# Kernel optimization log

Measured on AMD Instinct MI355X. Metric: run time of the kernel, lower is better.

The kernel has to match this reference:

```python
import jax, jax.numpy as jnp
import numpy as np

L = 28; D = 1024; HQ = 16; HKV = 8; HD = 128; G = HQ // HKV
FF = 3072; VOCAB = 151936; THETA = 1000000.0; EPS = 1e-6
B = 2; PAST = 1024
SCALE = HD ** -0.5


def _rmsnorm(x, w):
    v = jnp.mean(jnp.square(x), axis=-1, keepdims=True)
    return x * jax.lax.rsqrt(v + EPS) * w


def _rotate_half(x):
    x1, x2 = jnp.split(x, 2, axis=-1)
    return jnp.concatenate([-x2, x1], axis=-1)


def setup_inputs() -> dict:
    key = jax.random.key(0)
    ks = jax.random.split(key, 12)
    s = 0.02
    return {
        "input_embeds": jax.random.normal(ks[0], (B, 1, D), jnp.float32),
        "position_ids": jax.random.randint(ks[1], (B, 1), 0, PAST).astype(jnp.int32),
        "past_keys": jax.random.normal(ks[2], (L, B, HKV, PAST, HD), jnp.float32),
        "past_values": jax.random.normal(ks[3], (L, B, HKV, PAST, HD), jnp.float32),
        "Wq": s * jax.random.normal(ks[4], (L, D, HQ * HD), jnp.float32),
        "Wk": s * jax.random.normal(ks[5], (L, D, HKV * HD), jnp.float32),
        "Wv": s * jax.random.normal(ks[6], (L, D, HKV * HD), jnp.float32),
        "Wo": s * jax.random.normal(ks[7], (L, HQ * HD, D), jnp.float32),
        "Wg": s * jax.random.normal(ks[8], (L, D, FF), jnp.float32),
        "Wu": s * jax.random.normal(ks[9], (L, D, FF), jnp.float32),
        "Wd": s * jax.random.normal(ks[10], (L, FF, D), jnp.float32),
        "ln1_w": jnp.ones((L, D), jnp.float32),
        "ln2_w": jnp.ones((L, D), jnp.float32),
        "qn_w": jnp.ones((L, HD), jnp.float32),
        "kn_w": jnp.ones((L, HD), jnp.float32),
        "final_norm_w": jnp.ones((D,), jnp.float32),
        "lm_head_w": s * jax.random.normal(ks[11], (D, VOCAB), jnp.float32),
    }


def reference(input_embeds, position_ids, past_keys, past_values,
              Wq, Wk, Wv, Wo, Wg, Wu, Wd,
              ln1_w, ln2_w, qn_w, kn_w, final_norm_w, lm_head_w):
    # Rotary embeddings for the single new position.
    pos = position_ids.astype(jnp.float32)                      # [B,1]
    inv_freq = 1.0 / (THETA ** (jnp.arange(0, HD, 2, dtype=jnp.float32) / HD))
    freqs = pos[..., None] * inv_freq                           # [B,1,HD/2]
    emb = jnp.concatenate([freqs, freqs], axis=-1)              # [B,1,HD]
    cos = jnp.cos(emb)[:, None, :, :]                           # [B,1,1,HD] (head bcast)
    sin = jnp.sin(emb)[:, None, :, :]

    def layer(h, xs):
        wq, wk, wv, wo, wg, wu, wd, l1, l2, qw, kw, pk, pv = xs
        n = _rmsnorm(h, l1)                                     # [B,1,D]
        q = _rmsnorm((n @ wq).reshape(B, 1, HQ, HD), qw).transpose(0, 2, 1, 3)   # [B,HQ,1,HD]
        k = _rmsnorm((n @ wk).reshape(B, 1, HKV, HD), kw).transpose(0, 2, 1, 3)  # [B,HKV,1,HD]
        v = (n @ wv).reshape(B, 1, HKV, HD).transpose(0, 2, 1, 3)
        q = q * cos + _rotate_half(q) * sin
        k = k * cos + _rotate_half(k) * sin
        K = jnp.concatenate([pk, k], axis=2)                    # [B,HKV,PAST+1,HD]
        V = jnp.concatenate([pv, v], axis=2)
        # GQA without materializing repeated KV: q heads grouped kv-major,
        # matching torch _repeat_kv head ordering (head = kv*G + g).
        qg = q[:, :, 0, :].reshape(B, HKV, G, HD)
        scores = jnp.einsum('bkgd,bksd->bkgs', qg, K) * SCALE
        w = jax.nn.softmax(scores.astype(jnp.float32), axis=-1).astype(q.dtype)
        o = jnp.einsum('bkgs,bksd->bkgd', w, V).reshape(B, 1, HQ * HD)
        h = h + o @ wo
        m = _rmsnorm(h, l2)
        h = h + (jax.nn.silu(m @ wg) * (m @ wu)) @ wd           # SwiGLU MLP
        return h, (K, V)

    xs = (Wq, Wk, Wv, Wo, Wg, Wu, Wd, ln1_w, ln2_w, qn_w, kn_w, past_keys, past_values)
    h, (present_keys, present_values) = jax.lax.scan(layer, input_embeds, xs)
    logits = _rmsnorm(h, final_norm_w) @ lm_head_w              # [B,1,VOCAB]
    return logits, present_keys, present_values
```

## Files before the change

### kernel.cpp

```cpp
#include <hip/hip_runtime.h>
#include <math.h>

#define NL 28
#define DIM 1024
#define NHQ 16
#define NHKV 8
#define HDIM 128
#define NG 2
#define NFF 3072
#define NVOCAB 151936
#define NB 2
#define NPAST 1024
#define NPTOT 1025
#define EPSF 1e-6f
#define QKSCALE 0.08838834764831845f
#define LOGTHETA 13.815510557964274f

#define SQKV 8
#define SCH 32

#define OFF_N1   0
#define OFF_H    2048
#define OFF_H1   4096
#define OFF_QKV  8192
#define OFF_AM   73728
#define OFF_AL   74752
#define OFF_AO   75776
#define OFF_WO   206848
#define OFF_G    223232
#define OFF_U    272384
#define OFF_WD   321536

#define PK_OFF ((size_t)NB*NVOCAB)
#define PV_OFF (PK_OFF + (size_t)NL*NB*NHKV*NPTOT*HDIM)

__global__ __launch_bounds__(256) void k0_init(const float* __restrict__ embeds,
    const float* __restrict__ ln1, float* __restrict__ ws)
{
  int tid = threadIdx.x;
  __shared__ float red[512];
  int d = tid*4;
  float4 v0 = *(const float4*)(embeds + d);
  float4 v1 = *(const float4*)(embeds + DIM + d);
  *(float4*)(ws + OFF_H + d) = v0;
  *(float4*)(ws + OFF_H + DIM + d) = v1;
  red[tid]     = v0.x*v0.x + v0.y*v0.y + v0.z*v0.z + v0.w*v0.w;
  red[256+tid] = v1.x*v1.x + v1.y*v1.y + v1.z*v1.z + v1.w*v1.w;
  __syncthreads();
  for (int off = 128; off > 0; off >>= 1) {
    if (tid < off) { red[tid] += red[tid+off]; red[256+tid] += red[256+tid+off]; }
    __syncthreads();
  }
  float r0 = rsqrtf(red[0]/DIM + EPSF);
  float r1 = rsqrtf(red[256]/DIM + EPSF);
  float4 w = *(const float4*)(ln1 + d);
  float4 n0 = make_float4(v0.x*r0*w.x, v0.y*r0*w.y, v0.z*r0*w.z, v0.w*r0*w.w);
  float4 n1 = make_float4(v1.x*r1*w.x, v1.y*r1*w.y, v1.z*r1*w.z, v1.w*r1*w.w);
  *(float4*)(ws + OFF_N1 + d) = n0;
  *(float4*)(ws + OFF_N1 + DIM + d) = n1;
}

__global__ __launch_bounds__(256) void k1_qkv(
    const float* __restrict__ Wq_, const float* __restrict__ Wk_,
    const float* __restrict__ Wv_, const float* __restrict__ ln1,
    float* __restrict__ ws, int l)
{
  int bx = blockIdx.x, by = blockIdx.y;
  int tid = threadIdx.x;
  __shared__ __align__(16) float sh[NB][128];
  __shared__ __align__(16) float red[256*9];

  int ct = tid & 15, rs = tid >> 4;
  int colg = bx*64 + ct*4;
  const float* W; int O; int wcol;
  if (bx < 32)      { W = Wq_; O = 2048; wcol = colg; }
  else if (bx < 48) { W = Wk_; O = 1024; wcol = colg - 2048; }
  else              { W = Wv_; O = 1024; wcol = colg - 3072; }
  int r0 = rs*8;
  const float* Wp = W + (size_t)l*DIM*O + (size_t)(by*128 + r0)*O + wcol;
  float4 wb[8];
  #pragma unroll
  for (int i = 0; i < 8; i++) wb[i] = *(const float4*)(Wp + (size_t)i*O);

  if (l == 0) {
    int b = tid >> 7, r = tid & 127;
    sh[b][r] = ws[OFF_N1 + b*DIM + by*128 + r];
    __syncthreads();
  } else {
    int d = tid*4;
    float4 a0 = *(const float4*)(ws + OFF_H1 + d);
    float4 a1 = *(const float4*)(ws + OFF_H1 + DIM + d);
    #pragma unroll
    for (int s = 0; s < 8; s++) {
      float4 p0 = *(const float4*)(ws + OFF_WD + (s*NB + 0)*DIM + d);
      float4 p1 = *(const float4*)(ws + OFF_WD + (s*NB + 1)*DIM + d);
      a0.x += p0.x; a0.y += p0.y; a0.z += p0.z; a0.w += p0.w;
      a1.x += p1.x; a1.y += p1.y; a1.z += p1.z; a1.w += p1.w;
    }
    if (bx == 0 && by == 0) {
      *(float4*)(ws + OFF_H + d) = a0;
      *(float4*)(ws + OFF_H + DIM + d) = a1;
    }
    red[tid]     = a0.x*a0.x + a0.y*a0.y + a0.z*a0.z + a0.w*a0.w;
    red[256+tid] = a1.x*a1.x + a1.y*a1.y + a1.z*a1.z + a1.w*a1.w;
    __syncthreads();
    for (int off = 128; off > 0; off >>= 1) {
      if (tid < off) { red[tid] += red[tid+off]; red[256+tid] += red[256+tid+off]; }
      __syncthreads();
    }
    float rq0 = rsqrtf(red[0]/DIM + EPSF);
    float rq1 = rsqrtf(red[256]/DIM + EPSF);
    float4 lw = *(const float4*)(ln1 + (size_t)l*DIM + d);
    int r = d - by*128;
    if (r >= 0 && r < 128) {
      sh[0][r] = a0.x*rq0*lw.x; sh[0][r+1] = a0.y*rq0*lw.y;
      sh[0][r+2] = a0.z*rq0*lw.z; sh[0][r+3] = a0.w*rq0*lw.w;
      sh[1][r] = a1.x*rq1*lw.x; sh[1][r+1] = a1.y*rq1*lw.y;
      sh[1][r+2] = a1.z*rq1*lw.z; sh[1][r+3] = a1.w*rq1*lw.w;
    }
    __syncthreads();
  }

  float a[2][4] = {};
  #pragma unroll
  for (int i = 0; i < 8; i++) {
    float x0 = sh[0][r0+i], x1 = sh[1][r0+i];
    a[0][0] += x0*wb[i].x; a[0][1] += x0*wb[i].y; a[0][2] += x0*wb[i].z; a[0][3] += x0*wb[i].w;
    a[1][0] += x1*wb[i].x; a[1][1] += x1*wb[i].y; a[1][2] += x1*wb[i].z; a[1][3] += x1*wb[i].w;
  }
  float* rp = red + tid*9;
  #pragma unroll
  for (int e = 0; e < 4; e++) { rp[e] = a[0][e]; rp[4+e] = a[1][e]; }
  __syncthreads();
  if (tid < 16) {
    float o[8] = {};
    #pragma unroll
    for (int j = 0; j < 16; j++) {
      const float* q = red + (size_t)(j*16 + tid)*9;
      #pragma unroll
      for (int e = 0; e < 8; e++) o[e] += q[e];
    }
    int cg = bx*64 + tid*4;
    #pragma unroll
    for (int e = 0; e < 4; e++) {
      ws[OFF_QKV + (by*NB + 0)*4096 + cg + e] = o[e];
      ws[OFF_QKV + (by*NB + 1)*4096 + cg + e] = o[4+e];
    }
  }
}

__global__ __launch_bounds__(256) void k2_attn(
    const float* __restrict__ pastK, const float* __restrict__ pastV,
    const int* __restrict__ posids, const float* __restrict__ qnw,
    const float* __restrict__ knw, float* __restrict__ out,
    float* __restrict__ ws, int l)
{
  int c = blockIdx.x, kv = blockIdx.y, b = blockIdx.z;
  int tid = threadIdx.x;
  __shared__ __align__(16) float qf[NG][HDIM];
  __shared__ __align__(16) float kf[HDIM];
  __shared__ __align__(16) float vf[HDIM];
  __shared__ __align__(16) float pre[3*HDIM];
  __shared__ __align__(16) float po[8][NG][HDIM];
  __shared__ float red[256];
  __shared__ float pm[8][NG], pl[8][NG];

  int g = tid >> 7, o = tid & 127;
  int hq = kv*NG + g;
  float qraw = 0.f, kvraw = 0.f;
  #pragma unroll
  for (int s = 0; s < SQKV; s++) qraw += ws[OFF_QKV + (s*NB + b)*4096 + hq*HDIM + o];
  if (g == 0) {
    #pragma unroll
    for (int s = 0; s < SQKV; s++) kvraw += ws[OFF_QKV + (s*NB + b)*4096 + 2048 + kv*HDIM + o];
  } else {
    #pragma unroll
    for (int s = 0; s < SQKV; s++) kvraw += ws[OFF_QKV + (s*NB + b)*4096 + 3072 + kv*HDIM + o];
  }
  red[tid] = qraw*qraw;
  __syncthreads();
  for (int off = 64; off > 0; off >>= 1) {
    if (o < off) red[tid] += red[tid+off];
    __syncthreads();
  }
  float qr = rsqrtf(red[g*128]/HDIM + EPSF);
  __syncthreads();
  red[tid] = (g == 0) ? kvraw*kvraw : 0.f;
  __syncthreads();
  for (int off = 128; off > 0; off >>= 1) {
    if (tid < off) red[tid] += red[tid+off];
    __syncthreads();
  }
  float kr = rsqrtf(red[0]/HDIM + EPSF);
  pre[g*HDIM + o] = qraw*qr*qnw[l*HDIM + o];
  if (g == 0) pre[2*HDIM + o] = kvraw*kr*knw[l*HDIM + o];
  else vf[o] = kvraw;
  __syncthreads();
  float pos = (float)posids[b];
  int j = o & 63;
  float ang = pos * expf(-(2.0f*(float)j/(float)HDIM)*LOGTHETA);
  float sn, cs;
  sincosf(ang, &sn, &cs);
  {
    float qv = pre[g*HDIM + o];
    float qo = (o < 64) ? -pre[g*HDIM + o + 64] : pre[g*HDIM + o - 64];
    qf[g][o] = qv*cs + qo*sn;
    if (g == 0) {
      float kx = pre[2*HDIM + o];
      float ko = (o < 64) ? -pre[2*HDIM + o + 64] : pre[2*HDIM + o - 64];
      kf[o] = kx*cs + ko*sn;
    }
  }
  __syncthreads();

  int lane = tid & 63, w = tid >> 6;
  int h = (lane >> 5) & 1, q = lane & 31;
  int grp = w*2 + h;
  int p0 = c*32;
  int p1 = (c == SCH-1) ? NPTOT : p0 + 32;
  size_t pastbase = ((((size_t)l*NB + b)*NHKV + kv)*NPAST)*HDIM;
  size_t presbase = ((((size_t)l*NB + b)*NHKV + kv)*NPTOT)*HDIM;
  float4 q0 = *(const float4*)&qf[0][q*4];
  float4 q1 = *(const float4*)&qf[1][q*4];
  float sc0[5], sc1[5];
  float4 vv[5];
  int ns = 0;
  for (int p = p0 + grp; p < p1; p += 8) {
    float4 k4, v4;
    if (p < NPAST) {
      k4 = *(const float4*)(pastK + pastbase + (size_t)p*HDIM + q*4);
      v4 = *(const float4*)(pastV + pastbase + (size_t)p*HDIM + q*4);
    } else {
      k4 = *(const float4*)&kf[q*4];
      v4 = *(const float4*)&vf[q*4];
    }
    *(float4*)(out + PK_OFF + presbase + (size_t)p*HDIM + q*4) = k4;
    *(float4*)(out + PV_OFF + presbase + (size_t)p*HDIM + q*4) = v4;
    float d0 = q0.x*k4.x + q0.y*k4.y + q0.z*k4.z + q0.w*k4.w;
    float d1 = q1.x*k4.x + q1.y*k4.y + q1.z*k4.z + q1.w*k4.w;
    #pragma unroll
    for (int off = 16; off > 0; off >>= 1) {
      d0 += __shfl_xor(d0, off);
      d1 += __shfl_xor(d1, off);
    }
    sc0[ns] = d0*QKSCALE; sc1[ns] = d1*QKSCALE; vv[ns] = v4; ns++;
  }
  float m0 = -1e30f, m1 = -1e30f;
  for (int i = 0; i < ns; i++) { m0 = fmaxf(m0, sc0[i]); m1 = fmaxf(m1, sc1[i]); }
  if (q == 0) { pm[grp][0] = m0; pm[grp][1] = m1; }
  __syncthreads();
  float M0 = -1e30f, M1 = -1e30f;
  #pragma unroll
  for (int i = 0; i < 8; i++) { M0 = fmaxf(M0, pm[i][0]); M1 = fmaxf(M1, pm[i][1]); }
  float l0 = 0.f, l1 = 0.f;
  float4 o0 = {0,0,0,0}, o1 = {0,0,0,0};
  for (int i = 0; i < ns; i++) {
    float w0 = __expf(sc0[i] - M0), w1 = __expf(sc1[i] - M1);
    l0 += w0; l1 += w1;
    o0.x += w0*vv[i].x; o0.y += w0*vv[i].y; o0.z += w0*vv[i].z; o0.w += w0*vv[i].w;
    o1.x += w1*vv[i].x; o1.y += w1*vv[i].y; o1.z += w1*vv[i].z; o1.w += w1*vv[i].w;
  }
  if (q == 0) { pl[grp][0] = l0; pl[grp][1] = l1; }
  *(float4*)&po[grp][0][q*4] = o0;
  *(float4*)&po[grp][1][q*4] = o1;
  __syncthreads();
  {
    int head = tid >> 7, dd = tid & 127;
    float acc = 0.f;
    #pragma unroll
    for (int i = 0; i < 8; i++) acc += po[i][head][dd];
    int base = ((b*NHKV + kv)*NG + head)*SCH + c;
    ws[OFF_AO + (size_t)base*HDIM + dd] = acc;
    if (dd == 0) {
      float ll = 0.f;
      #pragma unroll
      for (int i = 0; i < 8; i++) ll += pl[i][head];
      ws[OFF_AM + base] = (head ? M1 : M0);
      ws[OFF_AL + base] = ll;
    }
  }
}

__global__ __launch_bounds__(256) void k3_wo(const float* __restrict__ Wo_,
    float* __restrict__ ws, int l)
{
  int bx = blockIdx.x, by = blockIdx.y;
  int tid = threadIdx.x;
  __shared__ __align__(16) float x[NB][256];
  __shared__ float wf[NB][2][SCH];
  __shared__ float invL[NB][2];
  __shared__ __align__(16) float red[256*9];

  int ct = tid & 7, rs = tid >> 3;
  int col = bx*32 + ct*4;
  int r0 = rs*8;
  const float* Wp = Wo_ + (size_t)l*(NHQ*HDIM)*DIM + (size_t)(by*256 + r0)*DIM + col;
  float4 wb[8];
  #pragma unroll
  for (int i = 0; i < 8; i++) wb[i] = *(const float4*)(Wp + (size_t)i*DIM);

  if (tid < 4) {
    int b = tid >> 1, hh = tid & 1;
    int hb = b*16 + by*2 + hh;
    const float* mp = ws + OFF_AM + hb*SCH;
    const float* lp = ws + OFF_AL + hb*SCH;
    float M = -1e30f;
    for (int cc = 0; cc < SCH; cc++) M = fmaxf(M, mp[cc]);
    float L = 0.f;
    for (int cc = 0; cc < SCH; cc++) { float f = __expf(mp[cc]-M); wf[b][hh][cc] = f; L += lp[cc]*f; }
    invL[b][hh] = 1.0f/L;
  }
  __syncthreads();
  for (int e = tid; e < 512; e += 256) {
    int b = e >> 8, rr = e & 255, hh = rr >> 7, dd = rr & 127;
    int hb = b*16 + by*2 + hh;
    const float* op = ws + OFF_AO + (size_t)(hb*SCH)*HDIM + dd;
    float acc = 0.f;
    for (int cc = 0; cc < SCH; cc++) acc += op[(size_t)cc*HDIM]*wf[b][hh][cc];
    x[b][rr] = acc*invL[b][hh];
  }
  __syncthreads();
  float a[2][4] = {};
  #pragma unroll
  for (int i = 0; i < 8; i++) {
    float x0 = x[0][r0+i], x1 = x[1][r0+i];
    a[0][0] += x0*wb[i].x; a[0][1] += x0*wb[i].y; a[0][2] += x0*wb[i].z; a[0][3] += x0*wb[i].w;
    a[1][0] += x1*wb[i].x; a[1][1] += x1*wb[i].y; a[1][2] += x1*wb[i].z; a[1][3] += x1*wb[i].w;
  }
  float* rp = red + tid*9;
  #pragma unroll
  for (int e = 0; e < 4; e++) { rp[e] = a[0][e]; rp[4+e] = a[1][e]; }
  __syncthreads();
  if (tid < 8) {
    float o[8] = {};
    #pragma unroll
    for (int j = 0; j < 32; j++) {
      const float* qq = red + (size_t)(j*8 + tid)*9;
      #pragma unroll
      for (int e = 0; e < 8; e++) o[e] += qq[e];
    }
    int cg = bx*32 + tid*4;
    #pragma unroll
    for (int e = 0; e < 4; e++) {
      ws[OFF_WO + (by*NB + 0)*DIM + cg + e] = o[e];
      ws[OFF_WO + (by*NB + 1)*DIM + cg + e] = o[4+e];
    }
  }
}

__global__ __launch_bounds__(256) void k4_mlp1(const float* __restrict__ Wg_,
    const float* __restrict__ Wu_, const float* __restrict__ ln2,
    float* __restrict__ ws, int l)
{
  int bx = blockIdx.x, by = blockIdx.y;
  int tid = threadIdx.x;
  __shared__ __align__(16) float sh[NB][128];
  __shared__ __align__(16) float red[256*9];

  int ct = tid & 15, rs = tid >> 4;
  int col = bx*64 + ct*4;
  int r0 = rs*8;
  const float* Wgp = Wg_ + (size_t)l*DIM*NFF + (size_t)(by*128 + r0)*NFF + col;
  const float* Wup = Wu_ + (size_t)l*DIM*NFF + (size_t)(by*128 + r0)*NFF + col;
  float4 wg[8], wu[8];
  #pragma unroll
  for (int i = 0; i < 8; i++) {
    wg[i] = *(const float4*)(Wgp + (size_t)i*NFF);
    wu[i] = *(const float4*)(Wup + (size_t)i*NFF);
  }

  int d = tid*4;
  float4 a0 = *(const float4*)(ws + OFF_H + d);
  float4 a1 = *(const float4*)(ws + OFF_H + DIM + d);
  #pragma unroll
  for (int s = 0; s < 8; s++) {
    float4 p0 = *(const float4*)(ws + OFF_WO + (s*NB + 0)*DIM + d);
    float4 p1 = *(const float4*)(ws + OFF_WO + (s*NB + 1)*DIM + d);
    a0.x += p0.x; a0.y += p0.y; a0.z += p0.z; a0.w += p0.w;
    a1.x += p1.x; a1.y += p1.y; a1.z += p1.z; a1.w += p1.w;
  }
  if (bx == 0 && by == 0) {
    *(float4*)(ws + OFF_H1 + d) = a0;
    *(float4*)(ws + OFF_H1 + DIM + d) = a1;
  }
  red[tid]     = a0.x*a0.x + a0.y*a0.y + a0.z*a0.z + a0.w*a0.w;
  red[256+tid] = a1.x*a1.x + a1.y*a1.y + a1.z*a1.z + a1.w*a1.w;
  __syncthreads();
  for (int off = 128; off > 0; off >>= 1) {
    if (tid < off) { red[tid] += red[tid+off]; red[256+tid] += red[256+tid+off]; }
    __syncthreads();
  }
  float rq0 = rsqrtf(red[0]/DIM + EPSF);
  float rq1 = rsqrtf(red[256]/DIM + EPSF);
  float4 lw = *(const float4*)(ln2 + (size_t)l*DIM + d);
  int r = d - by*128;
  if (r >= 0 && r < 128) {
    sh[0][r] = a0.x*rq0*lw.x; sh[0][r+1] = a0.y*rq0*lw.y;
    sh[0][r+2] = a0.z*rq0*lw.z; sh[0][r+3] = a0.w*rq0*lw.w;
    sh[1][r] = a1.x*rq1*lw.x; sh[1][r+1] = a1.y*rq1*lw.y;
    sh[1][r+2] = a1.z*rq1*lw.z; sh[1][r+3] = a1.w*rq1*lw.w;
  }
  __syncthreads();

  float ag[2][4] = {}, au[2][4] = {};
  #pragma unroll
  for (int i = 0; i < 8; i++) {
    float x0 = sh[0][r0+i], x1 = sh[1][r0+i];
    ag[0][0] += x0*wg[i].x; ag[0][1] += x0*wg[i].y; ag[0][2] += x0*wg[i].z; ag[0][3] += x0*wg[i].w;
    ag[1][0] += x1*wg[i].x; ag[1][1] += x1*wg[i].y; ag[1][2] += x1*wg[i].z; ag[1][3] += x1*wg[i].w;
    au[0][0] += x0*wu[i].x; au[0][1] += x0*wu[i].y; au[0][2] += x0*wu[i].z; au[0][3] += x0*wu[i].w;
    au[1][0] += x1*wu[i].x; au[1][1] += x1*wu[i].y; au[1][2] += x1*wu[i].z; au[1][3] += x1*wu[i].w;
  }
  float* rp = red + tid*9;
  #pragma unroll
  for (int e = 0; e < 4; e++) { rp[e] = ag[0][e]; rp[4+e] = ag[1][e]; }
  __syncthreads();
  if (tid < 16) {
    float o[8] = {};
    #pragma unroll
    for (int j = 0; j < 16; j++) {
      const float* qq = red + (size_t)(j*16 + tid)*9;
      #pragma unroll
      for (int e = 0; e < 8; e++) o[e] += qq[e];
    }
    int cg = bx*64 + tid*4;
    #pragma unroll
    for (int e = 0; e < 4; e++) {
      ws[OFF_G + (by*NB + 0)*NFF + cg + e] = o[e];
      ws[OFF_G + (by*NB + 1)*NFF + cg + e] = o[4+e];
    }
  }
  __syncthreads();
  #pragma unroll
  for (int e = 0; e < 4; e++) { rp[e] = au[0][e]; rp[4+e] = au[1][e]; }
  __syncthreads();
  if (tid < 16) {
    float o[8] = {};
    #pragma unroll
    for (int j = 0; j < 16; j++) {
      const float* qq = red + (size_t)(j*16 + tid)*9;
      #pragma unroll
      for (int e = 0; e < 8; e++) o[e] += qq[e];
    }
    int cg = bx*64 + tid*4;
    #pragma unroll
    for (int e = 0; e < 4; e++) {
      ws[OFF_U + (by*NB + 0)*NFF + cg + e] = o[e];
      ws[OFF_U + (by*NB + 1)*NFF + cg + e] = o[4+e];
    }
  }
}

__global__ __launch_bounds__(256) void k5_mlp2(const float* __restrict__ Wd_,
    float* __restrict__ ws, int l)
{
  int bx = blockIdx.x, by = blockIdx.y;
  int tid = threadIdx.x;
  __shared__ __align__(16) float act[NB][384];
  __shared__ __align__(16) float red[256*9];

  int ct = tid & 7, rs = tid >> 3;
  int col = bx*32 + ct*4;
  int r0 = rs*12;
  const float* Wp = Wd_ + (size_t)l*NFF*DIM + (size_t)(by*384 + r0)*DIM + col;
  float4 wb[12];
  #pragma unroll
  for (int i = 0; i < 12; i++) wb[i] = *(const float4*)(Wp + (size_t)i*DIM);

  for (int e = tid; e < 768; e += 256) {
    int b = (e >= 384);
    int loc = e - b*384;
    int ff = by*384 + loc;
    float g = 0.f, u = 0.f;
    #pragma unroll
    for (int s = 0; s < 8; s++) {
      g += ws[OFF_G + (s*NB + b)*NFF + ff];
      u += ws[OFF_U + (s*NB + b)*NFF + ff];
    }
    act[b][loc] = (g / (1.0f + __expf(-g)))*u;
  }
  __syncthreads();
  float a[2][4] = {};
  #pragma unroll
  for (int i = 0; i < 12; i++) {
    float x0 = act[0][r0+i], x1 = act[1][r0+i];
    a[0][0] += x0*wb[i].x; a[0][1] += x0*wb[i].y; a[0][2] += x0*wb[i].z; a[0][3] += x0*wb[i].w;
    a[1][0] += x1*wb[i].x; a[1][1] += x1*wb[i].y; a[1][2] += x1*wb[i].z; a[1][3] += x1*wb[i].w;
  }
  float* rp = red + tid*9;
  #pragma unroll
  for (int e = 0; e < 4; e++) { rp[e] = a[0][e]; rp[4+e] = a[1][e]; }
  __syncthreads();
  if (tid < 8) {
    float o[8] = {};
    #pragma unroll
    for (int j = 0; j < 32; j++) {
      const float* qq = red + (size_t)(j*8 + tid)*9;
      #pragma unroll
      for (int e = 0; e < 8; e++) o[e] += qq[e];
    }
    int cg = bx*32 + tid*4;
    #pragma unroll
    for (int e = 0; e < 4; e++) {
      ws[OFF_WD + (by*NB + 0)*DIM + cg + e] = o[e];
      ws[OFF_WD + (by*NB + 1)*DIM + cg + e] = o[4+e];
    }
  }
}

__global__ __launch_bounds__(256) void k6_lmhead(const float* __restrict__ lmw,
    const float* __restrict__ fnw, const float* __restrict__ ws,
    float* __restrict__ out)
{
  __shared__ __align__(16) float nf[NB*DIM];
  __shared__ __align__(16) float red[256*9];
  int tid = threadIdx.x;
  int d = tid*4;
  float4 a0 = *(const float4*)(ws + OFF_H1 + d);
  float4 a1 = *(const float4*)(ws + OFF_H1 + DIM + d);
  #pragma unroll
  for (int s = 0; s < 8; s++) {
    float4 p0 = *(const float4*)(ws + OFF_WD + (s*NB + 0)*DIM + d);
    float4 p1 = *(const float4*)(ws + OFF_WD + (s*NB + 1)*DIM + d);
    a0.x += p0.x; a0.y += p0.y; a0.z += p0.z; a0.w += p0.w;
    a1.x += p1.x; a1.y += p1.y; a1.z += p1.z; a1.w += p1.w;
  }
  red[tid]     = a0.x*a0.x + a0.y*a0.y + a0.z*a0.z + a0.w*a0.w;
  red[256+tid] = a1.x*a1.x + a1.y*a1.y + a1.z*a1.z + a1.w*a1.w;
  __syncthreads();
  for (int off = 128; off > 0; off >>= 1) {
    if (tid < off) { red[tid] += red[tid+off]; red[256+tid] += red[256+tid+off]; }
    __syncthreads();
  }
  float rq0 = rsqrtf(red[0]/DIM + EPSF);
  float rq1 = rsqrtf(red[256]/DIM + EPSF);
  float4 fw = *(const float4*)(fnw + d);
  nf[d]   = a0.x*rq0*fw.x; nf[d+1] = a0.y*rq0*fw.y;
  nf[d+2] = a0.z*rq0*fw.z; nf[d+3] = a0.w*rq0*fw.w;
  nf[DIM+d]   = a1.x*rq1*fw.x; nf[DIM+d+1] = a1.y*rq1*fw.y;
  nf[DIM+d+2] = a1.z*rq1*fw.z; nf[DIM+d+3] = a1.w*rq1*fw.w;
  __syncthreads();

  int ct = tid & 15, rs = tid >> 4;
  int col = blockIdx.x*64 + ct*4;
  const float* Wp = lmw + (size_t)(rs*64)*NVOCAB + col;
  float a[2][4] = {};
  for (int t = 0; t < 8; t++) {
    float4 wb[8];
    #pragma unroll
    for (int i = 0; i < 8; i++)
      wb[i] = *(const float4*)(Wp + (size_t)(t*8 + i)*NVOCAB);
    #pragma unroll
    for (int i = 0; i < 8; i++) {
      int rr = rs*64 + t*8 + i;
      float x0 = nf[rr], x1 = nf[DIM+rr];
      a[0][0] += x0*wb[i].x; a[0][1] += x0*wb[i].y; a[0][2] += x0*wb[i].z; a[0][3] += x0*wb[i].w;
      a[1][0] += x1*wb[i].x; a[1][1] += x1*wb[i].y; a[1][2] += x1*wb[i].z; a[1][3] += x1*wb[i].w;
    }
  }
  float* rp = red + tid*9;
  #pragma unroll
  for (int e = 0; e < 4; e++) { rp[e] = a[0][e]; rp[4+e] = a[1][e]; }
  __syncthreads();
  if (tid < 16) {
    float o[8] = {};
    #pragma unroll
    for (int j = 0; j < 16; j++) {
      const float* qq = red + (size_t)(j*16 + tid)*9;
      #pragma unroll
      for (int e = 0; e < 8; e++) o[e] += qq[e];
    }
    int cg = blockIdx.x*64 + tid*4;
    #pragma unroll
    for (int e = 0; e < 4; e++) {
      out[cg + e] = o[e];
      out[NVOCAB + cg + e] = o[4+e];
    }
  }
}

extern "C" void kernel_launch(void* const* d_in, const int* in_sizes, int n_in,
                              void* d_out, int out_size, void* d_ws, size_t ws_size,
                              hipStream_t stream) {
  (void)in_sizes; (void)n_in; (void)out_size; (void)ws_size;
  const float* embeds = (const float*)d_in[0];
  const int*   posids = (const int*)d_in[1];
  const float* pastK  = (const float*)d_in[2];
  const float* pastV  = (const float*)d_in[3];
  const float* Wq     = (const float*)d_in[4];
  const float* Wk     = (const float*)d_in[5];
  const float* Wv     = (const float*)d_in[6];
  const float* Wo     = (const float*)d_in[7];
  const float* Wg     = (const float*)d_in[8];
  const float* Wu     = (const float*)d_in[9];
  const float* Wd     = (const float*)d_in[10];
  const float* ln1    = (const float*)d_in[11];
  const float* ln2    = (const float*)d_in[12];
  const float* qnw    = (const float*)d_in[13];
  const float* knw    = (const float*)d_in[14];
  const float* fnw    = (const float*)d_in[15];
  const float* lmw    = (const float*)d_in[16];
  float* out = (float*)d_out;
  float* ws  = (float*)d_ws;

  k0_init<<<1, 256, 0, stream>>>(embeds, ln1, ws);
  for (int l = 0; l < NL; l++) {
    k1_qkv <<<dim3(64, 8), 256, 0, stream>>>(Wq, Wk, Wv, ln1, ws, l);
    k2_attn<<<dim3(SCH, NHKV, NB), 256, 0, stream>>>(pastK, pastV, posids, qnw, knw, out, ws, l);
    k3_wo  <<<dim3(32, 8), 256, 0, stream>>>(Wo, ws, l);
    k4_mlp1<<<dim3(48, 8), 256, 0, stream>>>(Wg, Wu, ln2, ws, l);
    k5_mlp2<<<dim3(32, 8), 256, 0, stream>>>(Wd, ws, l);
  }
  k6_lmhead<<<NVOCAB/64, 256, 0, stream>>>(lmw, fnw, ws, out);
}
```

Before: 1.470 ms.

## Use wave-shuffle reductions and hoist loads ahead of reductions in all kernels

Replaces the shared-memory tree reductions in the RMSNorm prologues with wave shuffle reductions plus a small cross-wave step, cutting the number of block barriers. Weight, KV-cache and partial-sum loads are issued before the reductions and pinned there with scheduling barriers, so global memory latency overlaps the norm computation. The attention combine is parallelised across lanes with shuffles instead of four serial threads, and the MLP activation gather is vectorised with float4. This raises register pressure from the hoisted loads, which could lower occupancy.

```diff
diff --git a/kernel.cpp b/kernel.cpp
--- a/kernel.cpp
+++ b/kernel.cpp
@@ -34,28 +34,32 @@
 #define PK_OFF ((size_t)NB*NVOCAB)
 #define PV_OFF (PK_OFF + (size_t)NL*NB*NHKV*NPTOT*HDIM)
 
+__device__ __forceinline__ float wave_red_sum(float v) {
+  #pragma unroll
+  for (int off = 32; off > 0; off >>= 1) v += __shfl_xor(v, off);
+  return v;
+}
+
 __global__ __launch_bounds__(256) void k0_init(const float* __restrict__ embeds,
     const float* __restrict__ ln1, float* __restrict__ ws)
 {
   int tid = threadIdx.x;
-  __shared__ float red[512];
+  int lane = tid & 63, w = tid >> 6;
+  __shared__ float wr[8];
   int d = tid*4;
   float4 v0 = *(const float4*)(embeds + d);
   float4 v1 = *(const float4*)(embeds + DIM + d);
+  float4 lw = *(const float4*)(ln1 + d);
   *(float4*)(ws + OFF_H + d) = v0;
   *(float4*)(ws + OFF_H + DIM + d) = v1;
-  red[tid]     = v0.x*v0.x + v0.y*v0.y + v0.z*v0.z + v0.w*v0.w;
-  red[256+tid] = v1.x*v1.x + v1.y*v1.y + v1.z*v1.z + v1.w*v1.w;
-  __syncthreads();
-  for (int off = 128; off > 0; off >>= 1) {
-    if (tid < off) { red[tid] += red[tid+off]; red[256+tid] += red[256+tid+off]; }
-    __syncthreads();
-  }
-  float r0 = rsqrtf(red[0]/DIM + EPSF);
-  float r1 = rsqrtf(red[256]/DIM + EPSF);
-  float4 w = *(const float4*)(ln1 + d);
-  float4 n0 = make_float4(v0.x*r0*w.x, v0.y*r0*w.y, v0.z*r0*w.z, v0.w*r0*w.w);
-  float4 n1 = make_float4(v1.x*r1*w.x, v1.y*r1*w.y, v1.z*r1*w.z, v1.w*r1*w.w);
+  float s0 = wave_red_sum(v0.x*v0.x + v0.y*v0.y + v0.z*v0.z + v0.w*v0.w);
+  float s1 = wave_red_sum(v1.x*v1.x + v1.y*v1.y + v1.z*v1.z + v1.w*v1.w);
+  if (lane == 0) { wr[w] = s0; wr[4+w] = s1; }
+  __syncthreads();
+  float r0 = rsqrtf((wr[0]+wr[1]+wr[2]+wr[3])/DIM + EPSF);
+  float r1 = rsqrtf((wr[4]+wr[5]+wr[6]+wr[7])/DIM + EPSF);
+  float4 n0 = make_float4(v0.x*r0*lw.x, v0.y*r0*lw.y, v0.z*r0*lw.z, v0.w*r0*lw.w);
+  float4 n1 = make_float4(v1.x*r1*lw.x, v1.y*r1*lw.y, v1.z*r1*lw.z, v1.w*r1*lw.w);
   *(float4*)(ws + OFF_N1 + d) = n0;
   *(float4*)(ws + OFF_N1 + DIM + d) = n1;
 }
@@ -67,8 +71,10 @@
 {
   int bx = blockIdx.x, by = blockIdx.y;
   int tid = threadIdx.x;
+  int lane = tid & 63, w = tid >> 6;
   __shared__ __align__(16) float sh[NB][128];
   __shared__ __align__(16) float red[256*9];
+  __shared__ float wr[8];
 
   int ct = tid & 15, rs = tid >> 4;
   int colg = bx*64 + ct*4;
@@ -79,12 +85,14 @@
   int r0 = rs*8;
   const float* Wp = W + (size_t)l*DIM*O + (size_t)(by*128 + r0)*O + wcol;
   float4 wb[8];
-  #pragma unroll
-  for (int i = 0; i < 8; i++) wb[i] = *(const float4*)(Wp + (size_t)i*O);
 
   if (l == 0) {
     int b = tid >> 7, r = tid & 127;
-    sh[b][r] = ws[OFF_N1 + b*DIM + by*128 + r];
+    float nv = ws[OFF_N1 + b*DIM + by*128 + r];
+    __builtin_amdgcn_sched_barrier(0);
+    #pragma unroll
+    for (int i = 0; i < 8; i++) wb[i] = *(const float4*)(Wp + (size_t)i*O);
+    sh[b][r] = nv;
     __syncthreads();
   } else {
     int d = tid*4;
@@ -97,20 +105,20 @@
       a0.x += p0.x; a0.y += p0.y; a0.z += p0.z; a0.w += p0.w;
       a1.x += p1.x; a1.y += p1.y; a1.z += p1.z; a1.w += p1.w;
     }
+    float4 lw = *(const float4*)(ln1 + (size_t)l*DIM + d);
+    __builtin_amdgcn_sched_barrier(0);
+    #pragma unroll
+    for (int i = 0; i < 8; i++) wb[i] = *(const float4*)(Wp + (size_t)i*O);
     if (bx == 0 && by == 0) {
       *(float4*)(ws + OFF_H + d) = a0;
       *(float4*)(ws + OFF_H + DIM + d) = a1;
     }
-    red[tid]     = a0.x*a0.x + a0.y*a0.y + a0.z*a0.z + a0.w*a0.w;
-    red[256+tid] = a1.x*a1.x + a1.y*a1.y + a1.z*a1.z + a1.w*a1.w;
+    float s0 = wave_red_sum(a0.x*a0.x + a0.y*a0.y + a0.z*a0.z + a0.w*a0.w);
+    float s1 = wave_red_sum(a1.x*a1.x + a1.y*a1.y + a1.z*a1.z + a1.w*a1.w);
+    if (lane == 0) { wr[w] = s0; wr[4+w] = s1; }
     __syncthreads();
-    for (int off = 128; off > 0; off >>= 1) {
-      if (tid < off) { red[tid] += red[tid+off]; red[256+tid] += red[256+tid+off]; }
-      __syncthreads();
-    }
-    float rq0 = rsqrtf(red[0]/DIM + EPSF);
-    float rq1 = rsqrtf(red[256]/DIM + EPSF);
-    float4 lw = *(const float4*)(ln1 + (size_t)l*DIM + d);
+    float rq0 = rsqrtf((wr[0]+wr[1]+wr[2]+wr[3])/DIM + EPSF);
+    float rq1 = rsqrtf((wr[4]+wr[5]+wr[6]+wr[7])/DIM + EPSF);
     int r = d - by*128;
     if (r >= 0 && r < 128) {
       sh[0][r] = a0.x*rq0*lw.x; sh[0][r+1] = a0.y*rq0*lw.y;
@@ -157,83 +165,80 @@
 {
   int c = blockIdx.x, kv = blockIdx.y, b = blockIdx.z;
   int tid = threadIdx.x;
+  int lane = tid & 63, w = tid >> 6;
+  int g = tid >> 7, o = tid & 127;
   __shared__ __align__(16) float qf[NG][HDIM];
   __shared__ __align__(16) float kf[HDIM];
   __shared__ __align__(16) float vf[HDIM];
-  __shared__ __align__(16) float pre[3*HDIM];
+  __shared__ __align__(16) float pre[NG][HDIM];
+  __shared__ __align__(16) float kpre[HDIM];
   __shared__ __align__(16) float po[8][NG][HDIM];
-  __shared__ float red[256];
+  __shared__ float wr[8];
   __shared__ float pm[8][NG], pl[8][NG];
 
-  int g = tid >> 7, o = tid & 127;
   int hq = kv*NG + g;
-  float qraw = 0.f, kvraw = 0.f;
-  #pragma unroll
-  for (int s = 0; s < SQKV; s++) qraw += ws[OFF_QKV + (s*NB + b)*4096 + hq*HDIM + o];
-  if (g == 0) {
-    #pragma unroll
-    for (int s = 0; s < SQKV; s++) kvraw += ws[OFF_QKV + (s*NB + b)*4096 + 2048 + kv*HDIM + o];
-  } else {
-    #pragma unroll
-    for (int s = 0; s < SQKV; s++) kvraw += ws[OFF_QKV + (s*NB + b)*4096 + 3072 + kv*HDIM + o];
-  }
-  red[tid] = qraw*qraw;
-  __syncthreads();
-  for (int off = 64; off > 0; off >>= 1) {
-    if (o < off) red[tid] += red[tid+off];
-    __syncthreads();
-  }
-  float qr = rsqrtf(red[g*128]/HDIM + EPSF);
-  __syncthreads();
-  red[tid] = (g == 0) ? kvraw*kvraw : 0.f;
-  __syncthreads();
-  for (int off = 128; off > 0; off >>= 1) {
-    if (tid < off) red[tid] += red[tid+off];
-    __syncthreads();
-  }
-  float kr = rsqrtf(red[0]/HDIM + EPSF);
-  pre[g*HDIM + o] = qraw*qr*qnw[l*HDIM + o];
-  if (g == 0) pre[2*HDIM + o] = kvraw*kr*knw[l*HDIM + o];
-  else vf[o] = kvraw;
-  __syncthreads();
+  float qp = 0.f, kp = 0.f;
+  #pragma unroll
+  for (int s = 0; s < SQKV; s++) qp += ws[OFF_QKV + (s*NB + b)*4096 + hq*HDIM + o];
+  int kvslot = g ? 3072 : 2048;
+  #pragma unroll
+  for (int s = 0; s < SQKV; s++) kp += ws[OFF_QKV + (s*NB + b)*4096 + kvslot + kv*HDIM + o];
+  float qw_ = qnw[l*HDIM + o];
+  float kw_ = knw[l*HDIM + o];
   float pos = (float)posids[b];
-  int j = o & 63;
-  float ang = pos * expf(-(2.0f*(float)j/(float)HDIM)*LOGTHETA);
-  float sn, cs;
-  sincosf(ang, &sn, &cs);
-  {
-    float qv = pre[g*HDIM + o];
-    float qo = (o < 64) ? -pre[g*HDIM + o + 64] : pre[g*HDIM + o - 64];
-    qf[g][o] = qv*cs + qo*sn;
-    if (g == 0) {
-      float kx = pre[2*HDIM + o];
-      float ko = (o < 64) ? -pre[2*HDIM + o + 64] : pre[2*HDIM + o - 64];
-      kf[o] = kx*cs + ko*sn;
-    }
-  }
-  __syncthreads();
-
-  int lane = tid & 63, w = tid >> 6;
-  int h = (lane >> 5) & 1, q = lane & 31;
-  int grp = w*2 + h;
+  __builtin_amdgcn_sched_barrier(0);
+
+  int grp = tid >> 5, q = tid & 31;
   int p0 = c*32;
   int p1 = (c == SCH-1) ? NPTOT : p0 + 32;
   size_t pastbase = ((((size_t)l*NB + b)*NHKV + kv)*NPAST)*HDIM;
   size_t presbase = ((((size_t)l*NB + b)*NHKV + kv)*NPTOT)*HDIM;
+  float4 kk[5], vv[5];
+  int ns = 0;
+  for (int p = p0 + grp; p < p1; p += 8) {
+    if (p < NPAST) {
+      kk[ns] = *(const float4*)(pastK + pastbase + (size_t)p*HDIM + q*4);
+      vv[ns] = *(const float4*)(pastV + pastbase + (size_t)p*HDIM + q*4);
+    }
+    ns++;
+  }
+  __builtin_amdgcn_sched_barrier(0);
+
+  float sq = wave_red_sum(qp*qp);
+  float sk = wave_red_sum(kp*kp);
+  if (lane == 0) { wr[w] = sq; wr[4+w] = sk; }
+  __syncthreads();
+  float qss = wr[g<<1] + wr[(g<<1)+1];
+  float qr = rsqrtf(qss/HDIM + EPSF);
+  float kss = wr[4] + wr[5];
+  float kr = rsqrtf(kss/HDIM + EPSF);
+  float qn = qp*qr*qw_;
+  pre[g][o] = qn;
+  if (g == 0) kpre[o] = kp*kr*kw_;
+  else vf[o] = kp;
+  __syncthreads();
+  float ang = pos * expf(-(2.0f*(float)(o & 63)/(float)HDIM)*LOGTHETA);
+  float sn, cs;
+  sincosf(ang, &sn, &cs);
+  {
+    float rotq = (o < 64) ? -pre[g][o+64] : pre[g][o-64];
+    qf[g][o] = qn*cs + rotq*sn;
+    if (g == 0) {
+      float kx = kpre[o];
+      float rotk = (o < 64) ? -kpre[o+64] : kpre[o-64];
+      kf[o] = kx*cs + rotk*sn;
+    }
+  }
+  __syncthreads();
+
   float4 q0 = *(const float4*)&qf[0][q*4];
   float4 q1 = *(const float4*)&qf[1][q*4];
   float sc0[5], sc1[5];
-  float4 vv[5];
-  int ns = 0;
-  for (int p = p0 + grp; p < p1; p += 8) {
+  int i = 0;
+  for (int p = p0 + grp; p < p1; p += 8, i++) {
     float4 k4, v4;
-    if (p < NPAST) {
-      k4 = *(const float4*)(pastK + pastbase + (size_t)p*HDIM + q*4);
-      v4 = *(const float4*)(pastV + pastbase + (size_t)p*HDIM + q*4);
-    } else {
-      k4 = *(const float4*)&kf[q*4];
-      v4 = *(const float4*)&vf[q*4];
-    }
+    if (p < NPAST) { k4 = kk[i]; v4 = vv[i]; }
+    else { k4 = *(const float4*)&kf[q*4]; v4 = *(const float4*)&vf[q*4]; vv[i] = v4; }
     *(float4*)(out + PK_OFF + presbase + (size_t)p*HDIM + q*4) = k4;
     *(float4*)(out + PV_OFF + presbase + (size_t)p*HDIM + q*4) = v4;
     float d0 = q0.x*k4.x + q0.y*k4.y + q0.z*k4.z + q0.w*k4.w;
@@ -243,22 +248,22 @@
       d0 += __shfl_xor(d0, off);
       d1 += __shfl_xor(d1, off);
     }
-    sc0[ns] = d0*QKSCALE; sc1[ns] = d1*QKSCALE; vv[ns] = v4; ns++;
+    sc0[i] = d0*QKSCALE; sc1[i] = d1*QKSCALE;
   }
   float m0 = -1e30f, m1 = -1e30f;
-  for (int i = 0; i < ns; i++) { m0 = fmaxf(m0, sc0[i]); m1 = fmaxf(m1, sc1[i]); }
+  for (int j = 0; j < i; j++) { m0 = fmaxf(m0, sc0[j]); m1 = fmaxf(m1, sc1[j]); }
   if (q == 0) { pm[grp][0] = m0; pm[grp][1] = m1; }
   __syncthreads();
   float M0 = -1e30f, M1 = -1e30f;
   #pragma unroll
-  for (int i = 0; i < 8; i++) { M0 = fmaxf(M0, pm[i][0]); M1 = fmaxf(M1, pm[i][1]); }
+  for (int j = 0; j < 8; j++) { M0 = fmaxf(M0, pm[j][0]); M1 = fmaxf(M1, pm[j][1]); }
   float l0 = 0.f, l1 = 0.f;
   float4 o0 = {0,0,0,0}, o1 = {0,0,0,0};
-  for (int i = 0; i < ns; i++) {
-    float w0 = __expf(sc0[i] - M0), w1 = __expf(sc1[i] - M1);
+  for (int j = 0; j < i; j++) {
+    float w0 = __expf(sc0[j] - M0), w1 = __expf(sc1[j] - M1);
     l0 += w0; l1 += w1;
-    o0.x += w0*vv[i].x; o0.y += w0*vv[i].y; o0.z += w0*vv[i].z; o0.w += w0*vv[i].w;
-    o1.x += w1*vv[i].x; o1.y += w1*vv[i].y; o1.z += w1*vv[i].z; o1.w += w1*vv[i].w;
+    o0.x += w0*vv[j].x; o0.y += w0*vv[j].y; o0.z += w0*vv[j].z; o0.w += w0*vv[j].w;
+    o1.x += w1*vv[j].x; o1.y += w1*vv[j].y; o1.z += w1*vv[j].z; o1.w += w1*vv[j].w;
   }
   if (q == 0) { pl[grp][0] = l0; pl[grp][1] = l1; }
   *(float4*)&po[grp][0][q*4] = o0;
@@ -268,13 +273,13 @@
     int head = tid >> 7, dd = tid & 127;
     float acc = 0.f;
     #pragma unroll
-    for (int i = 0; i < 8; i++) acc += po[i][head][dd];
+    for (int j = 0; j < 8; j++) acc += po[j][head][dd];
     int base = ((b*NHKV + kv)*NG + head)*SCH + c;
     ws[OFF_AO + (size_t)base*HDIM + dd] = acc;
     if (dd == 0) {
       float ll = 0.f;
       #pragma unroll
-      for (int i = 0; i < 8; i++) ll += pl[i][head];
+      for (int j = 0; j < 8; j++) ll += pl[j][head];
       ws[OFF_AM + base] = (head ? M1 : M0);
       ws[OFF_AL + base] = ll;
     }
@@ -291,6 +296,23 @@
   __shared__ float invL[NB][2];
   __shared__ __align__(16) float red[256*9];
 
+  if (tid < 128) {
+    int b = tid >> 6, hh = (tid >> 5) & 1, cc = tid & 31;
+    int hb = b*16 + by*2 + hh;
+    float m  = ws[OFF_AM + hb*SCH + cc];
+    float ll = ws[OFF_AL + hb*SCH + cc];
+    float M = m;
+    #pragma unroll
+    for (int off = 16; off > 0; off >>= 1) M = fmaxf(M, __shfl_xor(M, off));
+    float f = __expf(m - M);
+    float Ls = ll*f;
+    #pragma unroll
+    for (int off = 16; off > 0; off >>= 1) Ls += __shfl_xor(Ls, off);
+    wf[b][hh][cc] = f;
+    if (cc == 0) invL[b][hh] = 1.0f/Ls;
+  }
+  __builtin_amdgcn_sched_barrier(0);
+
   int ct = tid & 7, rs = tid >> 3;
   int col = bx*32 + ct*4;
   int r0 = rs*8;
@@ -298,24 +320,14 @@
   float4 wb[8];
   #pragma unroll
   for (int i = 0; i < 8; i++) wb[i] = *(const float4*)(Wp + (size_t)i*DIM);
-
-  if (tid < 4) {
-    int b = tid >> 1, hh = tid & 1;
-    int hb = b*16 + by*2 + hh;
-    const float* mp = ws + OFF_AM + hb*SCH;
-    const float* lp = ws + OFF_AL + hb*SCH;
-    float M = -1e30f;
-    for (int cc = 0; cc < SCH; cc++) M = fmaxf(M, mp[cc]);
-    float L = 0.f;
-    for (int cc = 0; cc < SCH; cc++) { float f = __expf(mp[cc]-M); wf[b][hh][cc] = f; L += lp[cc]*f; }
-    invL[b][hh] = 1.0f/L;
-  }
-  __syncthreads();
+  __syncthreads();
+
   for (int e = tid; e < 512; e += 256) {
     int b = e >> 8, rr = e & 255, hh = rr >> 7, dd = rr & 127;
     int hb = b*16 + by*2 + hh;
     const float* op = ws + OFF_AO + (size_t)(hb*SCH)*HDIM + dd;
     float acc = 0.f;
+    #pragma unroll
     for (int cc = 0; cc < SCH; cc++) acc += op[(size_t)cc*HDIM]*wf[b][hh][cc];
     x[b][rr] = acc*invL[b][hh];
   }
@@ -354,8 +366,23 @@
 {
   int bx = blockIdx.x, by = blockIdx.y;
   int tid = threadIdx.x;
+  int lane = tid & 63, w = tid >> 6;
   __shared__ __align__(16) float sh[NB][128];
   __shared__ __align__(16) float red[256*9];
+  __shared__ float wr[8];
+
+  int d = tid*4;
+  float4 a0 = *(const float4*)(ws + OFF_H + d);
+  float4 a1 = *(const float4*)(ws + OFF_H + DIM + d);
+  #pragma unroll
+  for (int s = 0; s < 8; s++) {
+    float4 p0 = *(const float4*)(ws + OFF_WO + (s*NB + 0)*DIM + d);
+    float4 p1 = *(const float4*)(ws + OFF_WO + (s*NB + 1)*DIM + d);
+    a0.x += p0.x; a0.y += p0.y; a0.z += p0.z; a0.w += p0.w;
+    a1.x += p1.x; a1.y += p1.y; a1.z += p1.z; a1.w += p1.w;
+  }
+  float4 lw = *(const float4*)(ln2 + (size_t)l*DIM + d);
+  __builtin_amdgcn_sched_barrier(0);
 
   int ct = tid & 15, rs = tid >> 4;
   int col = bx*64 + ct*4;
@@ -369,30 +396,16 @@
     wu[i] = *(const float4*)(Wup + (size_t)i*NFF);
   }
 
-  int d = tid*4;
-  float4 a0 = *(const float4*)(ws + OFF_H + d);
-  float4 a1 = *(const float4*)(ws + OFF_H + DIM + d);
-  #pragma unroll
-  for (int s = 0; s < 8; s++) {
-    float4 p0 = *(const float4*)(ws + OFF_WO + (s*NB + 0)*DIM + d);
-    float4 p1 = *(const float4*)(ws + OFF_WO + (s*NB + 1)*DIM + d);
-    a0.x += p0.x; a0.y += p0.y; a0.z += p0.z; a0.w += p0.w;
-    a1.x += p1.x; a1.y += p1.y; a1.z += p1.z; a1.w += p1.w;
-  }
   if (bx == 0 && by == 0) {
     *(float4*)(ws + OFF_H1 + d) = a0;
     *(float4*)(ws + OFF_H1 + DIM + d) = a1;
   }
-  red[tid]     = a0.x*a0.x + a0.y*a0.y + a0.z*a0.z + a0.w*a0.w;
-  red[256+tid] = a1.x*a1.x + a1.y*a1.y + a1.z*a1.z + a1.w*a1.w;
-  __syncthreads();
-  for (int off = 128; off > 0; off >>= 1) {
-    if (tid < off) { red[tid] += red[tid+off]; red[256+tid] += red[256+tid+off]; }
-    __syncthreads();
-  }
-  float rq0 = rsqrtf(red[0]/DIM + EPSF);
-  float rq1 = rsqrtf(red[256]/DIM + EPSF);
-  float4 lw = *(const float4*)(ln2 + (size_t)l*DIM + d);
+  float s0 = wave_red_sum(a0.x*a0.x + a0.y*a0.y + a0.z*a0.z + a0.w*a0.w);
+  float s1 = wave_red_sum(a1.x*a1.x + a1.y*a1.y + a1.z*a1.z + a1.w*a1.w);
+  if (lane == 0) { wr[w] = s0; wr[4+w] = s1; }
+  __syncthreads();
+  float rq0 = rsqrtf((wr[0]+wr[1]+wr[2]+wr[3])/DIM + EPSF);
+  float rq1 = rsqrtf((wr[4]+wr[5]+wr[6]+wr[7])/DIM + EPSF);
   int r = d - by*128;
   if (r >= 0 && r < 128) {
     sh[0][r] = a0.x*rq0*lw.x; sh[0][r+1] = a0.y*rq0*lw.y;
@@ -459,6 +472,23 @@
   __shared__ __align__(16) float act[NB][384];
   __shared__ __align__(16) float red[256*9];
 
+  float4 gacc = {0,0,0,0}, uacc = {0,0,0,0};
+  int pb = 0, pf4 = 0;
+  if (tid < 192) {
+    pb = tid / 96; pf4 = tid % 96;
+    int f4 = (by*384)/4 + pf4;
+    const float4* Gp = (const float4*)(ws + OFF_G);
+    const float4* Up = (const float4*)(ws + OFF_U);
+    #pragma unroll
+    for (int s = 0; s < 8; s++) {
+      float4 g4 = Gp[(size_t)(s*NB + pb)*(NFF/4) + f4];
+      float4 u4 = Up[(size_t)(s*NB + pb)*(NFF/4) + f4];
+      gacc.x += g4.x; gacc.y += g4.y; gacc.z += g4.z; gacc.w += g4.w;
+      uacc.x += u4.x; uacc.y += u4.y; uacc.z += u4.z; uacc.w += u4.w;
+    }
+  }
+  __builtin_amdgcn_sched_barrier(0);
+
   int ct = tid & 7, rs = tid >> 3;
   int col = bx*32 + ct*4;
   int r0 = rs*12;
@@ -467,19 +497,16 @@
   #pragma unroll
   for (int i = 0; i < 12; i++) wb[i] = *(const float4*)(Wp + (size_t)i*DIM);
 
-  for (int e = tid; e < 768; e += 256) {
-    int b = (e >= 384);
-    int loc = e - b*384;
-    int ff = by*384 + loc;
-    float g = 0.f, u = 0.f;
-    #pragma unroll
-    for (int s = 0; s < 8; s++) {
-      g += ws[OFF_G + (s*NB + b)*NFF + ff];
-      u += ws[OFF_U + (s*NB + b)*NFF + ff];
-    }
-    act[b][loc] = (g / (1.0f + __expf(-g)))*u;
-  }
-  __syncthreads();
+  if (tid < 192) {
+    float4 r;
+    r.x = (gacc.x / (1.0f + __expf(-gacc.x)))*uacc.x;
+    r.y = (gacc.y / (1.0f + __expf(-gacc.y)))*uacc.y;
+    r.z = (gacc.z / (1.0f + __expf(-gacc.z)))*uacc.z;
+    r.w = (gacc.w / (1.0f + __expf(-gacc.w)))*uacc.w;
+    *(float4*)&act[pb][pf4*4] = r;
+  }
+  __syncthreads();
+
   float a[2][4] = {};
   #pragma unroll
   for (int i = 0; i < 12; i++) {
@@ -514,7 +541,10 @@
 {
   __shared__ __align__(16) float nf[NB*DIM];
   __shared__ __align__(16) float red[256*9];
+  __shared__ float wr[8];
   int tid = threadIdx.x;
+  int lane = tid & 63, w = tid >> 6;
+
   int d = tid*4;
   float4 a0 = *(const float4*)(ws + OFF_H1 + d);
   float4 a1 = *(const float4*)(ws + OFF_H1 + DIM + d);
@@ -525,16 +555,15 @@
     a0.x += p0.x; a0.y += p0.y; a0.z += p0.z; a0.w += p0.w;
     a1.x += p1.x; a1.y += p1.y; a1.z += p1.z; a1.w += p1.w;
   }
-  red[tid]     = a0.x*a0.x + a0.y*a0.y + a0.z*a0.z + a0.w*a0.w;
-  red[256+tid] = a1.x*a1.x + a1.y*a1.y + a1.z*a1.z + a1.w*a1.w;
-  __syncthreads();
-  for (int off = 128; off > 0; off >>= 1) {
-    if (tid < off) { red[tid] += red[tid+off]; red[256+tid] += red[256+tid+off]; }
-    __syncthreads();
-  }
-  float rq0 = rsqrtf(red[0]/DIM + EPSF);
-  float rq1 = rsqrtf(red[256]/DIM + EPSF);
   float4 fw = *(const float4*)(fnw + d);
+  __builtin_amdgcn_sched_barrier(0);
+
+  float s0 = wave_red_sum(a0.x*a0.x + a0.y*a0.y + a0.z*a0.z + a0.w*a0.w);
+  float s1 = wave_red_sum(a1.x*a1.x + a1.y*a1.y + a1.z*a1.z + a1.w*a1.w);
+  if (lane == 0) { wr[w] = s0; wr[4+w] = s1; }
+  __syncthreads();
+  float rq0 = rsqrtf((wr[0]+wr[1]+wr[2]+wr[3])/DIM + EPSF);
+  float rq1 = rsqrtf((wr[4]+wr[5]+wr[6]+wr[7])/DIM + EPSF);
   nf[d]   = a0.x*rq0*fw.x; nf[d+1] = a0.y*rq0*fw.y;
   nf[d+2] = a0.z*rq0*fw.z; nf[d+3] = a0.w*rq0*fw.w;
   nf[DIM+d]   = a1.x*rq1*fw.x; nf[DIM+d+1] = a1.y*rq1*fw.y;
```

After: 1.406 ms. -4.4%, faster.
